# Kernel optimization log

Measured on AMD Instinct MI355X. Metric: run time of the kernel, lower is better.

## Reference

```python
import jax, jax.numpy as jnp
import numpy as np

H = 64        # hidden_dim
HEADS = 4
HD = H // HEADS

def setup_inputs() -> dict:
    key = jax.random.key(0)
    ks = jax.random.split(key, 32)
    def w(k, shape, fan_in):
        return jax.random.normal(k, shape, dtype=jnp.float32) * (1.0 / np.sqrt(fan_in))
    inp = {
        'robot_states': jax.random.normal(ks[0], (32, 512, 7), dtype=jnp.float32),
        'task_states': jax.random.normal(ks[1], (32, 128, 6), dtype=jnp.float32),
        # robot encoder: Linear(7,H) ReLU Linear(H,H) ReLU
        'r_w1': w(ks[2], (7, H), 7),  'r_b1': jnp.zeros((H,), jnp.float32),
        'r_w2': w(ks[3], (H, H), H),  'r_b2': jnp.zeros((H,), jnp.float32),
        # task encoder: Linear(6,H) ReLU Linear(H,H) ReLU
        't_w1': w(ks[4], (6, H), 6),  't_b1': jnp.zeros((H,), jnp.float32),
        't_w2': w(ks[5], (H, H), H),  't_b2': jnp.zeros((H,), jnp.float32),
        # MultiheadAttention (query=tasks, key/value=robots)
        'wq': w(ks[6], (H, H), H), 'bq': jnp.zeros((H,), jnp.float32),
        'wk': w(ks[7], (H, H), H), 'bk': jnp.zeros((H,), jnp.float32),
        'wv': w(ks[8], (H, H), H), 'bv': jnp.zeros((H,), jnp.float32),
        'wo': w(ks[9], (H, H), H), 'bo': jnp.zeros((H,), jnp.float32),
        # allocation net: Linear(2H,H) ReLU Linear(H,H//2) ReLU Linear(H//2,1)
        'a_w1': w(ks[10], (2 * H, H), 2 * H), 'a_b1': jnp.zeros((H,), jnp.float32),
        'a_w2': w(ks[11], (H, H // 2), H),    'a_b2': jnp.zeros((H // 2,), jnp.float32),
        'a_w3': w(ks[12], (H // 2, 1), H // 2), 'a_b3': jnp.zeros((1,), jnp.float32),
        'num_robots': 512,
        'num_tasks': 128,
    }
    return inp

def reference(robot_states, task_states, r_w1, r_b1, r_w2, r_b2,
              t_w1, t_b1, t_w2, t_b2, wq, bq, wk, bk, wv, bv, wo, bo,
              a_w1, a_b1, a_w2, a_b2, a_w3, a_b3, num_robots, num_tasks):
    relu = jax.nn.relu
    B = robot_states.shape[0]
    # encoders
    rf = relu(relu(robot_states @ r_w1 + r_b1) @ r_w2 + r_b2)[:, :num_robots]  # [B,R,H]
    tf = relu(relu(task_states @ t_w1 + t_b1) @ t_w2 + t_b2)[:, :num_tasks]    # [B,T,H]
    # multihead attention: tasks attend to robots
    q = (tf @ wq + bq).reshape(B, -1, HEADS, HD)
    k = (rf @ wk + bk).reshape(B, -1, HEADS, HD)
    v = (rf @ wv + bv).reshape(B, -1, HEADS, HD)
    logits = jnp.einsum('bthd,brhd->bhtr', q, k) / np.sqrt(HD)
    attn = jax.nn.softmax(logits, axis=-1)
    ctx = jnp.einsum('bhtr,brhd->bthd', attn, v).reshape(B, -1, H)
    tf = ctx @ wo + bo  # [B,T,H]
    # pairwise allocation MLP: concat([task, robot]) @ a_w1 split into two halves
    tp = tf @ a_w1[:H]   # [B,T,H]
    rp = rf @ a_w1[H:]   # [B,R,H]
    h1 = relu(tp[:, :, None, :] + rp[:, None, :, :] + a_b1)  # [B,T,R,H]
    h2 = relu(h1 @ a_w2 + a_b2)                              # [B,T,R,H//2]
    scores = (h2 @ a_w3)[..., 0] + a_b3[0]                   # [B,T,R]
    return jax.nn.softmax(scores, axis=-1)
```

## Files before the change

kernel.cpp:

```cpp
#include <hip/hip_runtime.h>
#include <hip/hip_bf16.h>
#include <math.h>

#define NB 32
#define NR 512
#define NT 128

typedef __attribute__((ext_vector_type(8))) short short8;
typedef __attribute__((ext_vector_type(4))) float f32x4;
typedef __attribute__((ext_vector_type(2))) float f32x2;

__device__ __forceinline__ float wred_max(float v){
#pragma unroll
  for (int o = 32; o > 0; o >>= 1) v = fmaxf(v, __shfl_xor(v, o));
  return v;
}
__device__ __forceinline__ float wred_sum(float v){
#pragma unroll
  for (int o = 32; o > 0; o >>= 1) v += __shfl_xor(v, o);
  return v;
}
__device__ __forceinline__ float dot4(float4 a, float4 b){
  return a.x * b.x + a.y * b.y + a.z * b.z + a.w * b.w;
}

__device__ __forceinline__ float dpp_add16(float s){
  int x;
  x = __builtin_amdgcn_update_dpp(0, __float_as_int(s), 0x111, 0xf, 0xf, true);
  s += __int_as_float(x);
  x = __builtin_amdgcn_update_dpp(0, __float_as_int(s), 0x112, 0xf, 0xf, true);
  s += __int_as_float(x);
  x = __builtin_amdgcn_update_dpp(0, __float_as_int(s), 0x114, 0xf, 0xf, true);
  s += __int_as_float(x);
  x = __builtin_amdgcn_update_dpp(0, __float_as_int(s), 0x118, 0xf, 0xf, true);
  s += __int_as_float(x);
  return s;
}

__global__ __launch_bounds__(256) void enc_kernel(
    const float* __restrict__ rs, const float* __restrict__ ts,
    const float* __restrict__ r_w1, const float* __restrict__ r_b1,
    const float* __restrict__ r_w2, const float* __restrict__ r_b2,
    const float* __restrict__ t_w1, const float* __restrict__ t_b1,
    const float* __restrict__ t_w2, const float* __restrict__ t_b2,
    const float* __restrict__ wq, const float* __restrict__ bq,
    const float* __restrict__ wk, const float* __restrict__ bk,
    const float* __restrict__ wv, const float* __restrict__ bv,
    const float* __restrict__ a_w1, const float* __restrict__ a_w2,
    float* __restrict__ kbuf, float* __restrict__ vbuf,
    float* __restrict__ rpbuf, float* __restrict__ qbuf,
    unsigned short* __restrict__ w2f)
{
  __shared__ float w1s[448];
  __shared__ float wss[4096];
  __shared__ float h_s[32 * 66];
  __shared__ float rf_s[32 * 66];

  const int tid = threadIdx.x;
  const int blk = blockIdx.x;

  if (blk == 640) {
    if (tid < 64) {
      int l = tid, n16 = l & 15, g = l >> 4;
      for (int f = 0; f < 8; ++f) {
        int ntile = f & 1, ks = (f >> 1) & 1, part = f >> 2;
        for (int j = 0; j < 8; ++j) {
          int k = ks * 32 + g * 8 + j;
          int n = ntile * 16 + n16;
          unsigned wb = __float_as_uint(a_w2[k * 32 + n]);
          unsigned hib = wb & 0xffff0000u;
          float lof = __uint_as_float(wb) - __uint_as_float(hib);
          unsigned lob = __float_as_uint(lof) & 0xffff0000u;
          w2f[((size_t)f * 64 + l) * 8 + j] =
              (unsigned short)((part == 0 ? hib : lob) >> 16);
        }
      }
    }
    return;
  }

  const int rb = tid >> 3, t8 = tid & 7;
  const bool robot = blk < 512;

  if (robot) {
    if (tid < 112) ((float4*)w1s)[tid] = ((const float4*)r_w1)[tid];
#pragma unroll
    for (int c = 0; c < 4; ++c)
      ((float4*)wss)[c * 256 + tid] = ((const float4*)r_w2)[c * 256 + tid];
  } else {
    if (tid < 96) ((float4*)w1s)[tid] = ((const float4*)t_w1)[tid];
#pragma unroll
    for (int c = 0; c < 4; ++c)
      ((float4*)wss)[c * 256 + tid] = ((const float4*)t_w2)[c * 256 + tid];
  }

  int g, K1;
  const float* xin; const float* b1; const float* b2;
  if (robot) { g = blk * 32 + rb;          K1 = 7; xin = rs + (size_t)g * 7; b1 = r_b1; b2 = r_b2; }
  else       { g = (blk - 512) * 32 + rb;  K1 = 6; xin = ts + (size_t)g * 6; b1 = t_b1; b2 = t_b2; }

  float x[7];
  for (int k = 0; k < K1; ++k) x[k] = xin[k];
  __syncthreads();

  {
    float acc[8];
#pragma unroll
    for (int jj = 0; jj < 8; ++jj) acc[jj] = b1[t8 * 8 + jj];
    for (int k = 0; k < K1; ++k) {
      float xv = x[k];
#pragma unroll
      for (int jj = 0; jj < 8; ++jj) acc[jj] += xv * w1s[k * 64 + t8 * 8 + jj];
    }
#pragma unroll
    for (int jj = 0; jj < 8; ++jj) h_s[rb * 66 + t8 * 8 + jj] = fmaxf(acc[jj], 0.f);
  }
  __syncthreads();

  {
    float acc[8];
#pragma unroll
    for (int jj = 0; jj < 8; ++jj) acc[jj] = b2[t8 * 8 + jj];
    for (int k = 0; k < 64; ++k) {
      float hv = h_s[rb * 66 + k];
      const float4* wr = (const float4*)(wss + k * 64 + t8 * 8);
#pragma unroll
      for (int j4 = 0; j4 < 2; ++j4) {
        float4 w = wr[j4];
        acc[j4 * 4 + 0] += hv * w.x; acc[j4 * 4 + 1] += hv * w.y;
        acc[j4 * 4 + 2] += hv * w.z; acc[j4 * 4 + 3] += hv * w.w;
      }
    }
#pragma unroll
    for (int jj = 0; jj < 8; ++jj) rf_s[rb * 66 + t8 * 8 + jj] = fmaxf(acc[jj], 0.f);
  }

  const float* wp[3]; const float* bp[3]; float* op[3]; int npass;
  if (robot) {
    wp[0] = wk; bp[0] = bk;      op[0] = kbuf;
    wp[1] = wv; bp[1] = bv;      op[1] = vbuf;
    wp[2] = a_w1 + 64 * 64; bp[2] = nullptr; op[2] = rpbuf;
    npass = 3;
  } else {
    wp[0] = wq; bp[0] = bq; op[0] = qbuf; npass = 1;
  }
  for (int p = 0; p < npass; ++p) {
    __syncthreads();
#pragma unroll
    for (int c = 0; c < 4; ++c)
      ((float4*)wss)[c * 256 + tid] = ((const float4*)wp[p])[c * 256 + tid];
    __syncthreads();
    float acc[8];
#pragma unroll
    for (int jj = 0; jj < 8; ++jj) acc[jj] = bp[p] ? bp[p][t8 * 8 + jj] : 0.f;
    for (int k = 0; k < 64; ++k) {
      float hv = rf_s[rb * 66 + k];
      const float4* wr = (const float4*)(wss + k * 64 + t8 * 8);
#pragma unroll
      for (int j4 = 0; j4 < 2; ++j4) {
        float4 w = wr[j4];
        acc[j4 * 4 + 0] += hv * w.x; acc[j4 * 4 + 1] += hv * w.y;
        acc[j4 * 4 + 2] += hv * w.z; acc[j4 * 4 + 3] += hv * w.w;
      }
    }
    float4* o4 = (float4*)(op[p] + (size_t)g * 64 + t8 * 8);
    o4[0] = make_float4(acc[0], acc[1], acc[2], acc[3]);
    o4[1] = make_float4(acc[4], acc[5], acc[6], acc[7]);
  }
}

#define LGS 520
__global__ __launch_bounds__(256, 4) void attn_kernel(
    const float* __restrict__ qbuf, const float* __restrict__ kbuf,
    const float* __restrict__ vbuf,
    const float* __restrict__ wo, const float* __restrict__ bo,
    const float* __restrict__ a_w1, const float* __restrict__ a_b1,
    float* __restrict__ tpbuf)
{
  __shared__ float qt_s[2 * 64];
  __shared__ float lg[2][4 * LGS];
  __shared__ float inv_s[8];
  __shared__ float cp[4][2 * 64];
  __shared__ float ctx_s[2 * 64];

  const int tid = threadIdx.x;
  const int jj = blockIdx.x & 31;
  const int b  = (jj & 7) * 4 + (jj >> 3);
  const int t0 = (blockIdx.x >> 5) * 2;

  if (tid < 32) {
    int tt = tid >> 4, i4 = tid & 15;
    float4 v = ((const float4*)(qbuf + (size_t)(b * NT + t0 + tt) * 64))[i4];
    v.x *= 0.25f; v.y *= 0.25f; v.z *= 0.25f; v.w *= 0.25f;
    ((float4*)qt_s)[tid] = v;
  }
  __syncthreads();

  {
    const int h = tid & 3;
    const int r0 = tid >> 2;
    const float4* q0 = (const float4*)(qt_s + h * 16);
    const float4* q1 = (const float4*)(qt_s + 64 + h * 16);
    float4 q0a = q0[0], q0b = q0[1], q0c = q0[2], q0d = q0[3];
    float4 q1a = q1[0], q1b = q1[1], q1c = q1[2], q1d = q1[3];
    const float* kb0 = kbuf + (size_t)b * NR * 64 + h * 16;
    for (int it = 0; it < 8; ++it) {
      int r = r0 + it * 64;
      const float4* k4 = (const float4*)(kb0 + (size_t)r * 64);
      float4 ka = k4[0], kb = k4[1], kc = k4[2], kd = k4[3];
      float s0 = dot4(q0a, ka) + dot4(q0b, kb) + dot4(q0c, kc) + dot4(q0d, kd);
      float s1 = dot4(q1a, ka) + dot4(q1b, kb) + dot4(q1c, kc) + dot4(q1d, kd);
      lg[0][h * LGS + r] = s0;
      lg[1][h * LGS + r] = s1;
    }
  }
  __syncthreads();

  {
    int w = tid >> 6, lane = tid & 63;
    for (int p = 0; p < 2; ++p) {
      int pr = w * 2 + p, tt = pr >> 2, hh = pr & 3;
      float* row = &lg[tt][hh * LGS];
      float v0[8];
#pragma unroll
      for (int u = 0; u < 8; ++u) v0[u] = row[u * 64 + lane];
      float m = v0[0];
#pragma unroll
      for (int u = 1; u < 8; ++u) m = fmaxf(m, v0[u]);
      m = wred_max(m);
      float s = 0.f;
#pragma unroll
      for (int u = 0; u < 8; ++u) {
        float e = expf(v0[u] - m);
        row[u * 64 + lane] = e;
        s += e;
      }
      s = wred_sum(s);
      if (lane == 0) inv_s[tt * 4 + hh] = 1.f / s;
    }
  }
  __syncthreads();

  {
    int od = tid & 63, ch = tid >> 6;
    int h = od >> 4, d = od & 15;
    float acc0 = 0.f, acc1 = 0.f;
    const float* vptr = vbuf + (size_t)b * NR * 64 + h * 16 + d;
#pragma unroll 4
    for (int u = 0; u < 128; ++u) {
      int r = ch * 128 + u;
      float vv = vptr[(size_t)r * 64];
      acc0 += lg[0][h * LGS + r] * vv;
      acc1 += lg[1][h * LGS + r] * vv;
    }
    cp[ch][od]      = acc0;
    cp[ch][64 + od] = acc1;
  }
  __syncthreads();
  if (tid < 128) {
    int od = tid & 63, h = od >> 4;
    ctx_s[tid] = (cp[0][tid] + cp[1][tid] + cp[2][tid] + cp[3][tid]) *
                 inv_s[(tid >> 6) * 4 + h];
  }
  __syncthreads();

  {
    int jd = tid & 63, kc = tid >> 6;
    float p0 = 0.f, p1 = 0.f;
    for (int k = 0; k < 16; ++k) {
      float w = wo[(kc * 16 + k) * 64 + jd];
      p0 += ctx_s[kc * 16 + k] * w;
      p1 += ctx_s[64 + kc * 16 + k] * w;
    }
    cp[kc][jd]      = p0;
    cp[kc][64 + jd] = p1;
  }
  __syncthreads();
  if (tid < 128) {
    int jd = tid & 63;
    qt_s[tid] = cp[0][tid] + cp[1][tid] + cp[2][tid] + cp[3][tid] + bo[jd];
  }
  __syncthreads();

  {
    int jd = tid & 63, kc = tid >> 6;
    float p0 = 0.f, p1 = 0.f;
    for (int k = 0; k < 16; ++k) {
      float w = a_w1[(kc * 16 + k) * 64 + jd];
      p0 += qt_s[kc * 16 + k] * w;
      p1 += qt_s[64 + kc * 16 + k] * w;
    }
    cp[kc][jd]      = p0;
    cp[kc][64 + jd] = p1;
  }
  __syncthreads();
  if (tid < 128) {
    int jd = tid & 63;
    tpbuf[(size_t)(b * NT + t0) * 64 + tid] =
        cp[0][tid] + cp[1][tid] + cp[2][tid] + cp[3][tid] + a_b1[jd];
  }
}

__device__ __forceinline__ void mk2(f32x2 r, f32x2 t,
                                    unsigned* h, unsigned* l)
{
  f32x2 x = r + t;
  x = __builtin_elementwise_max(x, (f32x2){0.f, 0.f});
  __hip_bfloat162 hb = __float22bfloat162_rn(make_float2(x.x, x.y));
  unsigned hh; __builtin_memcpy(&hh, &hb, 4);
  f32x2 hf;
  hf.x = __int_as_float((int)(hh << 16));
  hf.y = __int_as_float((int)(hh & 0xffff0000u));
  f32x2 e = x - hf;
  __hip_bfloat162 lb = __float22bfloat162_rn(make_float2(e.x, e.y));
  unsigned ll; __builtin_memcpy(&ll, &lb, 4);
  *h = hh; *l = ll;
}

__device__ __forceinline__ void mk_frags(float4 ra, float4 rb,
                                         float4 ta, float4 tb,
                                         short8* Ah, short8* Al)
{
  unsigned h0, h1, h2, h3, l0, l1, l2, l3;
  mk2((f32x2){ra.x, ra.y}, (f32x2){ta.x, ta.y}, &h0, &l0);
  mk2((f32x2){ra.z, ra.w}, (f32x2){ta.z, ta.w}, &h1, &l1);
  mk2((f32x2){rb.x, rb.y}, (f32x2){tb.x, tb.y}, &h2, &l2);
  mk2((f32x2){rb.z, rb.w}, (f32x2){tb.z, tb.w}, &h3, &l3);
  *Ah = __builtin_bit_cast(short8, make_int4((int)h0, (int)h1, (int)h2, (int)h3));
  *Al = __builtin_bit_cast(short8, make_int4((int)l0, (int)l1, (int)l2, (int)l3));
}

__global__ __launch_bounds__(256) void pair_kernel(
    const float* __restrict__ tpbuf, const float* __restrict__ rpbuf,
    const unsigned short* __restrict__ w2f,
    const float* __restrict__ a_b2, const float* __restrict__ a_w3,
    float* __restrict__ out)
{
  __shared__ float scores_s[2][512];
  __shared__ float red_a[4];
  __shared__ float red_b[4];

  const int tid = threadIdx.x;
  const int jj = blockIdx.x & 31;
  const int b  = (jj & 7) * 4 + (jj >> 3);
  const int t2 = blockIdx.x >> 5;
  const int wave = tid >> 6, lane = tid & 63;
  const int n16 = lane & 15, g = lane >> 4;

  short8 B[8];
#pragma unroll
  for (int f = 0; f < 8; ++f)
    B[f] = __builtin_bit_cast(short8, ((const int4*)w2f)[f * 64 + lane]);

  const float* tpA = tpbuf + (size_t)(b * NT + t2 * 2) * 64 + g * 8;
  const float* tpB = tpA + 64;
  float4 tA0a = *(const float4*)(tpA),      tA0b = *(const float4*)(tpA + 4);
  float4 tA1a = *(const float4*)(tpA + 32), tA1b = *(const float4*)(tpA + 36);
  float4 tB0a = *(const float4*)(tpB),      tB0b = *(const float4*)(tpB + 4);
  float4 tB1a = *(const float4*)(tpB + 32), tB1b = *(const float4*)(tpB + 36);

  float b20 = a_b2[n16], b21 = a_b2[16 + n16];
  float w30 = a_w3[n16], w31 = a_w3[16 + n16];

  const float* rpb = rpbuf + (size_t)b * NR * 64 + g * 8;

  const float4* rp0 = (const float4*)(rpb + (size_t)(wave * 128 + n16) * 64);
  float4 ra0 = rp0[0], rb0 = rp0[1], ra1 = rp0[8], rb1 = rp0[9];

#pragma unroll
  for (int mt = 0; mt < 8; ++mt) {
    float4 na0, nb0, na1, nb1;
    if (mt < 7) {
      const float4* rpn =
          (const float4*)(rpb + (size_t)(wave * 128 + (mt + 1) * 16 + n16) * 64);
      na0 = rpn[0]; nb0 = rpn[1]; na1 = rpn[8]; nb1 = rpn[9];
    }

#pragma unroll
    for (int task = 0; task < 2; ++task) {
      short8 Ah0, Al0, Ah1, Al1;
      if (task == 0) {
        mk_frags(ra0, rb0, tA0a, tA0b, &Ah0, &Al0);
        mk_frags(ra1, rb1, tA1a, tA1b, &Ah1, &Al1);
      } else {
        mk_frags(ra0, rb0, tB0a, tB0b, &Ah0, &Al0);
        mk_frags(ra1, rb1, tB1a, tB1b, &Ah1, &Al1);
      }
      f32x4 acc0 = (f32x4){b20, b20, b20, b20};
      f32x4 acc1 = (f32x4){b21, b21, b21, b21};
      acc0 = __builtin_amdgcn_mfma_f32_16x16x32_bf16(Ah0, B[0], acc0, 0, 0, 0);
      acc1 = __builtin_amdgcn_mfma_f32_16x16x32_bf16(Ah0, B[1], acc1, 0, 0, 0);
      acc0 = __builtin_amdgcn_mfma_f32_16x16x32_bf16(Al0, B[0], acc0, 0, 0, 0);
      acc1 = __builtin_amdgcn_mfma_f32_16x16x32_bf16(Al0, B[1], acc1, 0, 0, 0);
      acc0 = __builtin_amdgcn_mfma_f32_16x16x32_bf16(Ah0, B[4], acc0, 0, 0, 0);
      acc1 = __builtin_amdgcn_mfma_f32_16x16x32_bf16(Ah0, B[5], acc1, 0, 0, 0);
      acc0 = __builtin_amdgcn_mfma_f32_16x16x32_bf16(Ah1, B[2], acc0, 0, 0, 0);
      acc1 = __builtin_amdgcn_mfma_f32_16x16x32_bf16(Ah1, B[3], acc1, 0, 0, 0);
      acc0 = __builtin_amdgcn_mfma_f32_16x16x32_bf16(Al1, B[2], acc0, 0, 0, 0);
      acc1 = __builtin_amdgcn_mfma_f32_16x16x32_bf16(Al1, B[3], acc1, 0, 0, 0);
      acc0 = __builtin_amdgcn_mfma_f32_16x16x32_bf16(Ah1, B[6], acc0, 0, 0, 0);
      acc1 = __builtin_amdgcn_mfma_f32_16x16x32_bf16(Ah1, B[7], acc1, 0, 0, 0);
#pragma unroll
      for (int reg = 0; reg < 4; ++reg) {
        float s = fmaxf(acc0[reg], 0.f) * w30 + fmaxf(acc1[reg], 0.f) * w31;
        s = dpp_add16(s);
        if (n16 == 15)
          scores_s[task][wave * 128 + mt * 16 + g * 4 + reg] = s;
      }
    }
    ra0 = na0; rb0 = nb0; ra1 = na1; rb1 = nb1;
  }
  __syncthreads();

  const int lw = tid & 63, wid = tid >> 6;
  for (int task = 0; task < 2; ++task) {
    float s0 = scores_s[task][tid], s1 = scores_s[task][tid + 256];
    float mw = wred_max(fmaxf(s0, s1));
    if (lw == 0) red_a[wid] = mw;
    __syncthreads();
    float m = fmaxf(fmaxf(red_a[0], red_a[1]), fmaxf(red_a[2], red_a[3]));
    float e0 = expf(s0 - m), e1 = expf(s1 - m);
    float sw = wred_sum(e0 + e1);
    if (lw == 0) red_b[wid] = sw;
    __syncthreads();
    float inv = 1.f / (red_b[0] + red_b[1] + red_b[2] + red_b[3]);
    float* op = out + (size_t)(b * NT + t2 * 2 + task) * NR;
    op[tid]       = e0 * inv;
    op[256 + tid] = e1 * inv;
  }
}

extern "C" void kernel_launch(void* const* d_in, const int* in_sizes, int n_in,
                              void* d_out, int out_size, void* d_ws, size_t ws_size,
                              hipStream_t stream)
{
  const float* rs   = (const float*)d_in[0];
  const float* ts   = (const float*)d_in[1];
  const float* r_w1 = (const float*)d_in[2];  const float* r_b1 = (const float*)d_in[3];
  const float* r_w2 = (const float*)d_in[4];  const float* r_b2 = (const float*)d_in[5];
  const float* t_w1 = (const float*)d_in[6];  const float* t_b1 = (const float*)d_in[7];
  const float* t_w2 = (const float*)d_in[8];  const float* t_b2 = (const float*)d_in[9];
  const float* wq   = (const float*)d_in[10]; const float* bq   = (const float*)d_in[11];
  const float* wk   = (const float*)d_in[12]; const float* bk   = (const float*)d_in[13];
  const float* wv   = (const float*)d_in[14]; const float* bv   = (const float*)d_in[15];
  const float* wo   = (const float*)d_in[16]; const float* bo   = (const float*)d_in[17];
  const float* a_w1 = (const float*)d_in[18]; const float* a_b1 = (const float*)d_in[19];
  const float* a_w2 = (const float*)d_in[20]; const float* a_b2 = (const float*)d_in[21];
  const float* a_w3 = (const float*)d_in[22]; const float* a_b3 = (const float*)d_in[23];

  float* wsf   = (float*)d_ws;
  float* kbuf  = wsf;
  float* vbuf  = kbuf  + (size_t)NB * NR * 64;
  float* rpbuf = vbuf  + (size_t)NB * NR * 64;
  float* qbuf  = rpbuf + (size_t)NB * NR * 64;
  float* tpbuf = qbuf  + (size_t)NB * NT * 64;
  unsigned short* w2f = (unsigned short*)(tpbuf + (size_t)NB * NT * 64);

  enc_kernel<<<dim3(641), dim3(256), 0, stream>>>(
      rs, ts, r_w1, r_b1, r_w2, r_b2, t_w1, t_b1, t_w2, t_b2,
      wq, bq, wk, bk, wv, bv, a_w1, a_w2, kbuf, vbuf, rpbuf, qbuf, w2f);

  attn_kernel<<<dim3(2048), dim3(256), 0, stream>>>(
      qbuf, kbuf, vbuf, wo, bo, a_w1, a_b1, tpbuf);

  pair_kernel<<<dim3(2048), dim3(256), 0, stream>>>(
      tpbuf, rpbuf, w2f, a_b2, a_w3, (float*)d_out);
}
```

Measured before the change: 213.0 us.

## Fuse attention and pairwise allocation kernels into one launch

```diff
diff --git a/kernel.cpp b/kernel.cpp
--- a/kernel.cpp
+++ b/kernel.cpp
@@ -169,19 +169,55 @@
   }
 }
 
+__device__ __forceinline__ void mk2(f32x2 r, f32x2 t,
+                                    unsigned* h, unsigned* l)
+{
+  f32x2 x = r + t;
+  x = __builtin_elementwise_max(x, (f32x2){0.f, 0.f});
+  __hip_bfloat162 hb = __float22bfloat162_rn(make_float2(x.x, x.y));
+  unsigned hh; __builtin_memcpy(&hh, &hb, 4);
+  f32x2 hf;
+  hf.x = __int_as_float((int)(hh << 16));
+  hf.y = __int_as_float((int)(hh & 0xffff0000u));
+  f32x2 e = x - hf;
+  __hip_bfloat162 lb = __float22bfloat162_rn(make_float2(e.x, e.y));
+  unsigned ll; __builtin_memcpy(&ll, &lb, 4);
+  *h = hh; *l = ll;
+}
+
+__device__ __forceinline__ void mk_frags(float4 ra, float4 rb,
+                                         float4 ta, float4 tb,
+                                         short8* Ah, short8* Al)
+{
+  unsigned h0, h1, h2, h3, l0, l1, l2, l3;
+  mk2((f32x2){ra.x, ra.y}, (f32x2){ta.x, ta.y}, &h0, &l0);
+  mk2((f32x2){ra.z, ra.w}, (f32x2){ta.z, ta.w}, &h1, &l1);
+  mk2((f32x2){rb.x, rb.y}, (f32x2){tb.x, tb.y}, &h2, &l2);
+  mk2((f32x2){rb.z, rb.w}, (f32x2){tb.z, tb.w}, &h3, &l3);
+  *Ah = __builtin_bit_cast(short8, make_int4((int)h0, (int)h1, (int)h2, (int)h3));
+  *Al = __builtin_bit_cast(short8, make_int4((int)l0, (int)l1, (int)l2, (int)l3));
+}
+
 #define LGS 520
-__global__ __launch_bounds__(256, 4) void attn_kernel(
+__global__ __launch_bounds__(256, 4) void attn_pair_kernel(
     const float* __restrict__ qbuf, const float* __restrict__ kbuf,
     const float* __restrict__ vbuf,
     const float* __restrict__ wo, const float* __restrict__ bo,
     const float* __restrict__ a_w1, const float* __restrict__ a_b1,
-    float* __restrict__ tpbuf)
+    const unsigned short* __restrict__ w2f,
+    const float* __restrict__ a_b2, const float* __restrict__ a_w3,
+    const float* __restrict__ rpbuf,
+    float* __restrict__ out)
 {
   __shared__ float qt_s[2 * 64];
   __shared__ float lg[2][4 * LGS];
   __shared__ float inv_s[8];
   __shared__ float cp[4][2 * 64];
   __shared__ float ctx_s[2 * 64];
+  __shared__ float tp_f[2 * 64];
+  __shared__ float scores_s[2][512];
+  __shared__ float red_a[4];
+  __shared__ float red_b[4];
 
   const int tid = threadIdx.x;
   const int jj = blockIdx.x & 31;
@@ -296,54 +332,10 @@
   __syncthreads();
   if (tid < 128) {
     int jd = tid & 63;
-    tpbuf[(size_t)(b * NT + t0) * 64 + tid] =
-        cp[0][tid] + cp[1][tid] + cp[2][tid] + cp[3][tid] + a_b1[jd];
-  }
-}
-
-__device__ __forceinline__ void mk2(f32x2 r, f32x2 t,
-                                    unsigned* h, unsigned* l)
-{
-  f32x2 x = r + t;
-  x = __builtin_elementwise_max(x, (f32x2){0.f, 0.f});
-  __hip_bfloat162 hb = __float22bfloat162_rn(make_float2(x.x, x.y));
-  unsigned hh; __builtin_memcpy(&hh, &hb, 4);
-  f32x2 hf;
-  hf.x = __int_as_float((int)(hh << 16));
-  hf.y = __int_as_float((int)(hh & 0xffff0000u));
-  f32x2 e = x - hf;
-  __hip_bfloat162 lb = __float22bfloat162_rn(make_float2(e.x, e.y));
-  unsigned ll; __builtin_memcpy(&ll, &lb, 4);
-  *h = hh; *l = ll;
-}
-
-__device__ __forceinline__ void mk_frags(float4 ra, float4 rb,
-                                         float4 ta, float4 tb,
-                                         short8* Ah, short8* Al)
-{
-  unsigned h0, h1, h2, h3, l0, l1, l2, l3;
-  mk2((f32x2){ra.x, ra.y}, (f32x2){ta.x, ta.y}, &h0, &l0);
-  mk2((f32x2){ra.z, ra.w}, (f32x2){ta.z, ta.w}, &h1, &l1);
-  mk2((f32x2){rb.x, rb.y}, (f32x2){tb.x, tb.y}, &h2, &l2);
-  mk2((f32x2){rb.z, rb.w}, (f32x2){tb.z, tb.w}, &h3, &l3);
-  *Ah = __builtin_bit_cast(short8, make_int4((int)h0, (int)h1, (int)h2, (int)h3));
-  *Al = __builtin_bit_cast(short8, make_int4((int)l0, (int)l1, (int)l2, (int)l3));
-}
-
-__global__ __launch_bounds__(256) void pair_kernel(
-    const float* __restrict__ tpbuf, const float* __restrict__ rpbuf,
-    const unsigned short* __restrict__ w2f,
-    const float* __restrict__ a_b2, const float* __restrict__ a_w3,
-    float* __restrict__ out)
-{
-  __shared__ float scores_s[2][512];
-  __shared__ float red_a[4];
-  __shared__ float red_b[4];
-
-  const int tid = threadIdx.x;
-  const int jj = blockIdx.x & 31;
-  const int b  = (jj & 7) * 4 + (jj >> 3);
-  const int t2 = blockIdx.x >> 5;
+    tp_f[tid] = cp[0][tid] + cp[1][tid] + cp[2][tid] + cp[3][tid] + a_b1[jd];
+  }
+  __syncthreads();
+
   const int wave = tid >> 6, lane = tid & 63;
   const int n16 = lane & 15, g = lane >> 4;
 
@@ -352,8 +344,8 @@
   for (int f = 0; f < 8; ++f)
     B[f] = __builtin_bit_cast(short8, ((const int4*)w2f)[f * 64 + lane]);
 
-  const float* tpA = tpbuf + (size_t)(b * NT + t2 * 2) * 64 + g * 8;
-  const float* tpB = tpA + 64;
+  const float* tpA = tp_f + g * 8;
+  const float* tpB = tp_f + 64 + g * 8;
   float4 tA0a = *(const float4*)(tpA),      tA0b = *(const float4*)(tpA + 4);
   float4 tA1a = *(const float4*)(tpA + 32), tA1b = *(const float4*)(tpA + 36);
   float4 tB0a = *(const float4*)(tpB),      tB0b = *(const float4*)(tpB + 4);
@@ -424,7 +416,7 @@
     if (lw == 0) red_b[wid] = sw;
     __syncthreads();
     float inv = 1.f / (red_b[0] + red_b[1] + red_b[2] + red_b[3]);
-    float* op = out + (size_t)(b * NT + t2 * 2 + task) * NR;
+    float* op = out + (size_t)(b * NT + t0 + task) * NR;
     op[tid]       = e0 * inv;
     op[256 + tid] = e1 * inv;
   }
@@ -453,16 +445,13 @@
   float* vbuf  = kbuf  + (size_t)NB * NR * 64;
   float* rpbuf = vbuf  + (size_t)NB * NR * 64;
   float* qbuf  = rpbuf + (size_t)NB * NR * 64;
-  float* tpbuf = qbuf  + (size_t)NB * NT * 64;
-  unsigned short* w2f = (unsigned short*)(tpbuf + (size_t)NB * NT * 64);
+  unsigned short* w2f = (unsigned short*)(qbuf + (size_t)NB * NT * 64);
 
   enc_kernel<<<dim3(641), dim3(256), 0, stream>>>(
       rs, ts, r_w1, r_b1, r_w2, r_b2, t_w1, t_b1, t_w2, t_b2,
       wq, bq, wk, bk, wv, bv, a_w1, a_w2, kbuf, vbuf, rpbuf, qbuf, w2f);
 
-  attn_kernel<<<dim3(2048), dim3(256), 0, stream>>>(
-      qbuf, kbuf, vbuf, wo, bo, a_w1, a_b1, tpbuf);
-
-  pair_kernel<<<dim3(2048), dim3(256), 0, stream>>>(
-      tpbuf, rpbuf, w2f, a_b2, a_w3, (float*)d_out);
-}
+  attn_pair_kernel<<<dim3(2048), dim3(256), 0, stream>>>(
+      qbuf, kbuf, vbuf, wo, bo, a_w1, a_b1, w2f, a_b2, a_w3, rpbuf,
+      (float*)d_out);
+}
```

New measurement: 207.3 us. -2.7%, faster.
